# Performance work log

Measured on AMD Instinct MI355X. Metric: run time of the kernel, lower is better.

The kernel has to match this reference:

```python
import jax, jax.numpy as jnp
import numpy as np

N_NODES = 100000
N_EDGES = 1600000
IN_F = 128
OUT_F = 32
HEADS = 4
NEG_SLOPE = 0.2


def setup_inputs() -> dict:
    key = jax.random.key(0)
    k1, k2, k3, k4 = jax.random.split(key, 4)
    h = jax.random.normal(k1, (N_NODES, IN_F), dtype=jnp.float32)
    edge_index = jax.random.randint(k2, (2, N_EDGES), 0, N_NODES, dtype=jnp.int32)
    # xavier-ish scale for W [in, heads*out] and a [1, H, 2F]
    w_scale = 1.414 * (2.0 / (IN_F + HEADS * OUT_F)) ** 0.5
    a_scale = 1.414 * (2.0 / (1 + 2 * OUT_F)) ** 0.5
    W = jax.random.normal(k3, (IN_F, HEADS * OUT_F), dtype=jnp.float32) * w_scale
    a = jax.random.normal(k4, (1, HEADS, 2 * OUT_F), dtype=jnp.float32) * a_scale
    return {"h": h, "edge_index": edge_index, "W": W, "a": a}


def reference(h, edge_index, W, a):
    N = h.shape[0]
    Wh = (h @ W).reshape(N, HEADS, OUT_F)            # [N, H, F]
    # split attention vector: cat([Wh_src, Wh_dst]) . a == Wh_src.a_src + Wh_dst.a_dst
    a_src, a_dst = a[..., :OUT_F], a[..., OUT_F:]    # [1, H, F] each
    s_src = jnp.sum(Wh * a_src, axis=-1)             # [N, H] per-node src score
    s_dst = jnp.sum(Wh * a_dst, axis=-1)             # [N, H] per-node dst score
    src, dst = edge_index[0], edge_index[1]
    scores = jax.nn.leaky_relu(s_src[src] + s_dst[dst], NEG_SLOPE)  # [E, H]
    # scatter per-edge scores to a dense [N, H] table (-inf where no edge),
    # softmax over the NODE axis (dim 0, as in the torch code), gather back
    node_scores = jax.ops.segment_max(scores, dst, num_segments=N)  # [N, H], -inf empty
    attn = jax.nn.softmax(node_scores, axis=0)[dst]  # [E, H]
    # weighted scatter-add aggregation (dropout is identity in eval)
    out = jax.ops.segment_sum(attn[:, :, None] * Wh[src], dst, num_segments=N)
    return out.reshape(N, HEADS * OUT_F)
```

## Files before the change

### kernel.cpp

```cpp
#include <hip/hip_runtime.h>
#include <hip/hip_bf16.h>
#include <float.h>

#define N_NODES 100000
#define N_EDGES 1600000
#define HEADS 4
#define OUT_F 32
#define NEG_SLOPE 0.2f
#define EXP_SHIFT 8.0f

#define NB 391
#define NT 391
#define SCAP 12288

typedef __attribute__((ext_vector_type(8))) short short8;
typedef __attribute__((ext_vector_type(4))) float f32x4;

__device__ __forceinline__ int enc_f(float f) {
    int b = __float_as_int(f);
    return b >= 0 ? b : b ^ 0x7fffffff;
}
__device__ __forceinline__ float dec_f(int b) {
    return __int_as_float(b >= 0 ? b : b ^ 0x7fffffff);
}
#define ENC_NEG_FLT_MAX ((int)0x80800000)

__device__ __forceinline__ unsigned short f2bf(float f) {
    unsigned int u = __float_as_uint(f);
    u += 0x7fff + ((u >> 16) & 1);
    return (unsigned short)(u >> 16);
}

__global__ void k_wt(const float* __restrict__ W, unsigned short* __restrict__ Wt,
                     float* __restrict__ S) {
    if (blockIdx.x == 0 && threadIdx.x < 4) S[threadIdx.x] = 0.0f;
    int n = threadIdx.x;
    int k2 = blockIdx.x;
    float w0 = W[(size_t)(2 * k2) * 128 + n];
    float w1 = W[(size_t)(2 * k2 + 1) * 128 + n];
    ushort2 p = make_ushort2(f2bf(w0), f2bf(w1));
    *(ushort2*)&Wt[(size_t)n * 128 + 2 * k2] = p;
}

__global__ __launch_bounds__(256) void k_gemm(const float* __restrict__ hp,
                                              const unsigned short* __restrict__ Wt,
                                              const float* __restrict__ av,
                                              unsigned short* __restrict__ Whb,
                                              float* __restrict__ s_src,
                                              float* __restrict__ s_dst) {
    __shared__ short hs[64][136];
    __shared__ short wsB[128][136];
    int tid = threadIdx.x;
    int rowBase = blockIdx.x * 64;

    const short8* Wt8 = (const short8*)Wt;
#pragma unroll
    for (int i = 0; i < 8; i++) {
        int idx = tid + 256 * i;
        int n = idx >> 4, ch = idx & 15;
        *(short8*)&wsB[n][ch * 8] = Wt8[idx];
    }
    const float4* h4 = (const float4*)hp;
#pragma unroll
    for (int i = 0; i < 8; i++) {
        int idx = tid + 256 * i;
        int r = idx >> 5, c4 = idx & 31;
        int gr = rowBase + r;
        float4 v = (gr < N_NODES) ? h4[(size_t)gr * 32 + c4]
                                  : make_float4(0.f, 0.f, 0.f, 0.f);
        ushort4 p = make_ushort4(f2bf(v.x), f2bf(v.y), f2bf(v.z), f2bf(v.w));
        *(ushort4*)&hs[r][c4 * 4] = p;
    }
    __syncthreads();

    int lane = tid & 63;
    int wv = tid >> 6;
    int l16 = lane & 15, quad = lane >> 4;
    int mbase = wv * 16;

    short8 afr[4];
#pragma unroll
    for (int k4 = 0; k4 < 4; k4++)
        afr[k4] = *(const short8*)&hs[mbase + l16][k4 * 32 + quad * 8];

    f32x4 acc[8];
#pragma unroll
    for (int nt = 0; nt < 8; nt++) {
        acc[nt] = (f32x4){0.f, 0.f, 0.f, 0.f};
#pragma unroll
        for (int k4 = 0; k4 < 4; k4++) {
            short8 b = *(const short8*)&wsB[nt * 16 + l16][k4 * 32 + quad * 8];
            acc[nt] = __builtin_amdgcn_mfma_f32_16x16x32_bf16(afr[k4], b, acc[nt], 0, 0, 0);
        }
    }

    int row0 = rowBase + mbase + quad * 4;
#pragma unroll
    for (int r = 0; r < 4; r++) {
        int row = row0 + r;
        if (row < N_NODES) {
#pragma unroll
            for (int nt = 0; nt < 8; nt++)
                Whb[(size_t)row * 128 + nt * 16 + l16] = f2bf(acc[nt][r]);
        }
    }

    float ps[4][4], pd[4][4];
#pragma unroll
    for (int h = 0; h < 4; h++) {
        float a0s = av[h * 64 + l16];
        float a1s = av[h * 64 + 16 + l16];
        float a0d = av[h * 64 + 32 + l16];
        float a1d = av[h * 64 + 48 + l16];
#pragma unroll
        for (int r = 0; r < 4; r++) {
            ps[h][r] = acc[2 * h][r] * a0s + acc[2 * h + 1][r] * a1s;
            pd[h][r] = acc[2 * h][r] * a0d + acc[2 * h + 1][r] * a1d;
        }
    }
#pragma unroll
    for (int h = 0; h < 4; h++)
#pragma unroll
        for (int r = 0; r < 4; r++) {
#pragma unroll
            for (int off = 1; off < 16; off <<= 1) {
                ps[h][r] += __shfl_xor(ps[h][r], off);
                pd[h][r] += __shfl_xor(pd[h][r], off);
            }
        }
    if (l16 < 4) {
#pragma unroll
        for (int r = 0; r < 4; r++) {
            int row = row0 + r;
            if (row < N_NODES) {
                float vs = (l16 == 0) ? ps[0][r] : (l16 == 1) ? ps[1][r]
                         : (l16 == 2) ? ps[2][r] : ps[3][r];
                float vd = (l16 == 0) ? pd[0][r] : (l16 == 1) ? pd[1][r]
                         : (l16 == 2) ? pd[2][r] : pd[3][r];
                s_src[row * 4 + l16] = vs;
                s_dst[row * 4 + l16] = vd;
            }
        }
    }
}

__global__ __launch_bounds__(256) void k_hist(const int* __restrict__ ei,
                                              int* __restrict__ hist) {
    __shared__ int lh[NB];
    int tid = threadIdx.x, tile = blockIdx.x;
    for (int b = tid; b < NB; b += 256) lh[b] = 0;
    __syncthreads();
    const int4* d4 = (const int4*)(ei + N_EDGES);
    int base4 = tile * 1024;
    for (int i = tid; i < 1024; i += 256) {
        int i4 = base4 + i;
        if (i4 < N_EDGES / 4) {
            int4 d = d4[i4];
            atomicAdd(&lh[d.x >> 8], 1);
            atomicAdd(&lh[d.y >> 8], 1);
            atomicAdd(&lh[d.z >> 8], 1);
            atomicAdd(&lh[d.w >> 8], 1);
        }
    }
    __syncthreads();
    for (int b = tid; b < NB; b += 256) hist[tile * NB + b] = lh[b];
}

__global__ __launch_bounds__(512) void k_scan(const int* __restrict__ hist,
                                              int* __restrict__ tileoff,
                                              int* __restrict__ bin_total) {
    int b = blockIdx.x, tid = threadIdx.x;
    int val = (tid < NT) ? hist[tid * NB + b] : 0;
    int lane = tid & 63, wv = tid >> 6;
    int v = val;
#pragma unroll
    for (int off = 1; off < 64; off <<= 1) {
        int t = __shfl_up(v, off);
        if (lane >= off) v += t;
    }
    __shared__ int wtot[8], woff[8];
    if (lane == 63) wtot[wv] = v;
    __syncthreads();
    if (tid == 0) { int s = 0; for (int i = 0; i < 8; i++) { woff[i] = s; s += wtot[i]; } }
    __syncthreads();
    int incl = v + woff[wv];
    if (tid < NT) tileoff[tid * NB + b] = incl - val;
    if (tid == NT - 1) bin_total[b] = incl;
}

__global__ __launch_bounds__(512) void k_scan2(const int* __restrict__ bin_total,
                                               int* __restrict__ bin_start) {
    int tid = threadIdx.x;
    int val = (tid < NB) ? bin_total[tid] : 0;
    int lane = tid & 63, wv = tid >> 6;
    int v = val;
#pragma unroll
    for (int off = 1; off < 64; off <<= 1) {
        int t = __shfl_up(v, off);
        if (lane >= off) v += t;
    }
    __shared__ int wtot[8], woff[8];
    if (lane == 63) wtot[wv] = v;
    __syncthreads();
    if (tid == 0) { int s = 0; for (int i = 0; i < 8; i++) { woff[i] = s; s += wtot[i]; } }
    __syncthreads();
    if (tid < NB) bin_start[tid] = v + woff[wv] - val;
}

__global__ __launch_bounds__(256) void k_scat(const int* __restrict__ ei,
                                              const int* __restrict__ tileoff,
                                              const int* __restrict__ bin_start,
                                              int* __restrict__ ebuf) {
    __shared__ int lcur[NB];
    int tid = threadIdx.x, tile = blockIdx.x;
    for (int b = tid; b < NB; b += 256) lcur[b] = bin_start[b] + tileoff[tile * NB + b];
    __syncthreads();
    const int4* s4 = (const int4*)ei;
    const int4* d4 = (const int4*)(ei + N_EDGES);
    int base4 = tile * 1024;
    for (int i = tid; i < 1024; i += 256) {
        int i4 = base4 + i;
        if (i4 < N_EDGES / 4) {
            int4 s = s4[i4];
            int4 d = d4[i4];
            int p;
            p = atomicAdd(&lcur[d.x >> 8], 1); ebuf[p] = s.x | ((d.x & 255) << 17);
            p = atomicAdd(&lcur[d.y >> 8], 1); ebuf[p] = s.y | ((d.y & 255) << 17);
            p = atomicAdd(&lcur[d.z >> 8], 1); ebuf[p] = s.z | ((d.z & 255) << 17);
            p = atomicAdd(&lcur[d.w >> 8], 1); ebuf[p] = s.w | ((d.w & 255) << 17);
        }
    }
}

__global__ __launch_bounds__(256) void k_bucket(const int* __restrict__ bin_start,
                                                const int* __restrict__ bin_total,
                                                int* __restrict__ ebuf,
                                                int* __restrict__ cnt,
                                                int* __restrict__ start,
                                                const float* __restrict__ s_src,
                                                const float* __restrict__ s_dst,
                                                float* __restrict__ expv,
                                                float* __restrict__ S) {
    __shared__ int stage[SCAP];
    __shared__ int lh[256];
    __shared__ int lcur[256];
    __shared__ int nm[4][256];
    __shared__ int wtot[4], woff[4];
    __shared__ float sred[4][4];
    int b = blockIdx.x, tid = threadIdx.x;
    int base = bin_start[b], total = bin_total[b];
    if (total > SCAP) total = SCAP;
    lh[tid] = 0;
    nm[0][tid] = ENC_NEG_FLT_MAX; nm[1][tid] = ENC_NEG_FLT_MAX;
    nm[2][tid] = ENC_NEG_FLT_MAX; nm[3][tid] = ENC_NEG_FLT_MAX;
    __syncthreads();
    for (int i = tid; i < total; i += 256) {
        int rec = ebuf[base + i];
        stage[i] = rec;
        atomicAdd(&lh[(rec >> 17) & 255], 1);
    }
    __syncthreads();
    int val = lh[tid];
    int lane = tid & 63, wv = tid >> 6;
    int v = val;
#pragma unroll
    for (int off = 1; off < 64; off <<= 1) {
        int t = __shfl_up(v, off);
        if (lane >= off) v += t;
    }
    if (lane == 63) wtot[wv] = v;
    __syncthreads();
    if (tid == 0) { int s = 0; for (int i = 0; i < 4; i++) { woff[i] = s; s += wtot[i]; } }
    __syncthreads();
    int gpos = base + v + woff[wv] - val;
    int node = b * 256 + tid;
    if (node < N_NODES) { cnt[node] = val; start[node] = gpos; }
    lcur[tid] = gpos;
    __syncthreads();
    for (int i = tid; i < total; i += 256) {
        int rec = stage[i];
        int src = rec & 0x1FFFF;
        int ld = (rec >> 17) & 255;
        int p = atomicAdd(&lcur[ld], 1);
        ebuf[p] = src;
        float4 sv = ((const float4*)s_src)[src];
        atomicMax(&nm[0][ld], enc_f(sv.x));
        atomicMax(&nm[1][ld], enc_f(sv.y));
        atomicMax(&nm[2][ld], enc_f(sv.z));
        atomicMax(&nm[3][ld], enc_f(sv.w));
    }
    __syncthreads();
    float4 e4 = make_float4(0.f, 0.f, 0.f, 0.f);
    if (node < N_NODES) {
        float4 d = ((const float4*)s_dst)[node];
        float x;
        x = dec_f(nm[0][tid]) + d.x; x = x > 0.f ? x : NEG_SLOPE * x; e4.x = __expf(x - EXP_SHIFT);
        x = dec_f(nm[1][tid]) + d.y; x = x > 0.f ? x : NEG_SLOPE * x; e4.y = __expf(x - EXP_SHIFT);
        x = dec_f(nm[2][tid]) + d.z; x = x > 0.f ? x : NEG_SLOPE * x; e4.z = __expf(x - EXP_SHIFT);
        x = dec_f(nm[3][tid]) + d.w; x = x > 0.f ? x : NEG_SLOPE * x; e4.w = __expf(x - EXP_SHIFT);
        ((float4*)expv)[node] = e4;
    }
#pragma unroll
    for (int off = 32; off; off >>= 1) {
        e4.x += __shfl_xor(e4.x, off);
        e4.y += __shfl_xor(e4.y, off);
        e4.z += __shfl_xor(e4.z, off);
        e4.w += __shfl_xor(e4.w, off);
    }
    if (lane == 0) { sred[wv][0] = e4.x; sred[wv][1] = e4.y; sred[wv][2] = e4.z; sred[wv][3] = e4.w; }
    __syncthreads();
    if (tid < 4)
        atomicAdd(&S[tid], sred[0][tid] + sred[1][tid] + sred[2][tid] + sred[3][tid]);
}

__global__ __launch_bounds__(256) void k_agg(const unsigned int* __restrict__ Whb32,
                                             const int* __restrict__ esrc,
                                             const int* __restrict__ start,
                                             const int* __restrict__ cnt,
                                             const float* __restrict__ expv,
                                             const float* __restrict__ S,
                                             float* __restrict__ out) {
    int node = (blockIdx.x * 256 + threadIdx.x) >> 6;
    if (node >= N_NODES) return;
    int lane = threadIdx.x & 63;
    int base = __builtin_amdgcn_readfirstlane(start[node]);
    int deg  = __builtin_amdgcn_readfirstlane(cnt[node]);
    const unsigned int* Wl = Whb32 + lane;
    float accx = 0.f, accy = 0.f;
    int i = 0;
    for (; i + 16 <= deg; i += 16) {
        unsigned int v[16];
#pragma unroll
        for (int j = 0; j < 16; j++) {
            int s = esrc[base + i + j];
            v[j] = Wl[(size_t)s * 64];
        }
#pragma unroll
        for (int j = 0; j < 16; j++) {
            accx += __uint_as_float(v[j] << 16);
            accy += __uint_as_float(v[j] & 0xffff0000u);
        }
    }
    for (; i + 4 <= deg; i += 4) {
        unsigned int v[4];
#pragma unroll
        for (int j = 0; j < 4; j++) {
            int s = esrc[base + i + j];
            v[j] = Wl[(size_t)s * 64];
        }
#pragma unroll
        for (int j = 0; j < 4; j++) {
            accx += __uint_as_float(v[j] << 16);
            accy += __uint_as_float(v[j] & 0xffff0000u);
        }
    }
    for (; i < deg; i++) {
        int s = esrc[base + i];
        unsigned int v = Wl[(size_t)s * 64];
        accx += __uint_as_float(v << 16);
        accy += __uint_as_float(v & 0xffff0000u);
    }
    int head = lane >> 4;
    float attn = expv[node * 4 + head] / S[head];
    ((float2*)out)[(size_t)node * 64 + lane] = make_float2(accx * attn, accy * attn);
}

extern "C" void kernel_launch(void* const* d_in, const int* in_sizes, int n_in,
                              void* d_out, int out_size, void* d_ws, size_t ws_size,
                              hipStream_t stream) {
    const float* h  = (const float*)d_in[0];
    const int*   ei = (const int*)d_in[1];
    const float* W  = (const float*)d_in[2];
    const float* a  = (const float*)d_in[3];
    float* out = (float*)d_out;

    char* ws = (char*)d_ws;
    unsigned short* Whb = (unsigned short*)(ws);
    float* s_src     = (float*)(ws + 25600000);
    float* s_dst     = (float*)(ws + 27200000);
    float* expv      = (float*)(ws + 28800000);
    int*   cnt       = (int*)  (ws + 30400000);
    int*   start     = (int*)  (ws + 30800000);
    int*   ebuf      = (int*)  (ws + 31200000);
    int*   hist      = (int*)  (ws + 37600000);
    int*   tileoff   = (int*)  (ws + 38211524);
    int*   bin_total = (int*)  (ws + 38823048);
    int*   bin_start = (int*)  (ws + 38824612);
    float* S         = (float*)(ws + 38826176);
    unsigned short* Wt = (unsigned short*)ebuf;

    k_wt<<<64, 128, 0, stream>>>(W, Wt, S);
    k_gemm<<<1563, 256, 0, stream>>>(h, Wt, a, Whb, s_src, s_dst);
    k_hist<<<NT, 256, 0, stream>>>(ei, hist);
    k_scan<<<NB, 512, 0, stream>>>(hist, tileoff, bin_total);
    k_scan2<<<1, 512, 0, stream>>>(bin_total, bin_start);
    k_scat<<<NT, 256, 0, stream>>>(ei, tileoff, bin_start, ebuf);
    k_bucket<<<NB, 256, 0, stream>>>(bin_start, bin_total, ebuf, cnt, start,
                                     s_src, s_dst, expv, S);
    k_agg<<<25000, 256, 0, stream>>>((const unsigned int*)Whb, ebuf, start, cnt, expv, S, out);
}
```

Measured before the change: 236.8 us.

## Fixed-capacity 128-node bins, fuse hist with W prep, pad neighbor lists

Edges are binned into 782 bins of 128 destination nodes, each at a fixed offset of PCAP slots, which removes the second global scan kernel. The histogram pass and the W transpose are fused into one launch. The GEMM now loads h straight into registers, with 128 rows per block. Each node's neighbor list is padded to a multiple of 4 using a dummy source (row N_NODES of Whb, which the GEMM now writes), so the aggregation drops its scalar tail loop. The costs are extra workspace and padding traffic, plus a risk of overflow if a bin holds more than PCAP edges or a node has more than SCAP.

```diff
diff --git a/kernel.cpp b/kernel.cpp
--- a/kernel.cpp
+++ b/kernel.cpp
@@ -9,9 +9,10 @@
 #define NEG_SLOPE 0.2f
 #define EXP_SHIFT 8.0f
 
-#define NB 391
+#define NB 782
 #define NT 391
-#define SCAP 12288
+#define PCAP 4096
+#define SCAP 3072
 
 typedef __attribute__((ext_vector_type(8))) short short8;
 typedef __attribute__((ext_vector_type(4))) float f32x4;
@@ -31,57 +32,79 @@
     return (unsigned short)(u >> 16);
 }
 
-__global__ void k_wt(const float* __restrict__ W, unsigned short* __restrict__ Wt,
-                     float* __restrict__ S) {
-    if (blockIdx.x == 0 && threadIdx.x < 4) S[threadIdx.x] = 0.0f;
-    int n = threadIdx.x;
-    int k2 = blockIdx.x;
-    float w0 = W[(size_t)(2 * k2) * 128 + n];
-    float w1 = W[(size_t)(2 * k2 + 1) * 128 + n];
-    ushort2 p = make_ushort2(f2bf(w0), f2bf(w1));
-    *(ushort2*)&Wt[(size_t)n * 128 + 2 * k2] = p;
-}
-
-__global__ __launch_bounds__(256) void k_gemm(const float* __restrict__ hp,
+__global__ __launch_bounds__(256) void k_prep(const int* __restrict__ ei,
+                                              const float* __restrict__ W,
+                                              unsigned short* __restrict__ Wt,
+                                              int* __restrict__ hist,
+                                              float* __restrict__ S) {
+    __shared__ int lh[NB];
+    int b = blockIdx.x, tid = threadIdx.x;
+    if (b < NT) {
+        for (int i = tid; i < NB; i += 256) lh[i] = 0;
+        __syncthreads();
+        const int4* d4 = (const int4*)(ei + N_EDGES);
+        int base4 = b * 1024;
+#pragma unroll
+        for (int it = 0; it < 4; it++) {
+            int i4 = base4 + tid + 256 * it;
+            if (i4 < N_EDGES / 4) {
+                int4 d = d4[i4];
+                atomicAdd(&lh[d.x >> 7], 1);
+                atomicAdd(&lh[d.y >> 7], 1);
+                atomicAdd(&lh[d.z >> 7], 1);
+                atomicAdd(&lh[d.w >> 7], 1);
+            }
+        }
+        __syncthreads();
+        for (int i = tid; i < NB; i += 256) hist[b * NB + i] = lh[i];
+    } else {
+        int idx = (b - NT) * 256 + tid;
+        int n = idx & 127, k2 = idx >> 7;
+        float w0 = W[(size_t)(2 * k2) * 128 + n];
+        float w1 = W[(size_t)(2 * k2 + 1) * 128 + n];
+        *(ushort2*)&Wt[(size_t)n * 128 + 2 * k2] = make_ushort2(f2bf(w0), f2bf(w1));
+        if (b == NT && tid < 4) S[tid] = 0.0f;
+    }
+}
+
+__global__ __launch_bounds__(512) void k_gemm(const float* __restrict__ hp,
                                               const unsigned short* __restrict__ Wt,
                                               const float* __restrict__ av,
                                               unsigned short* __restrict__ Whb,
                                               float* __restrict__ s_src,
                                               float* __restrict__ s_dst) {
-    __shared__ short hs[64][136];
     __shared__ short wsB[128][136];
     int tid = threadIdx.x;
-    int rowBase = blockIdx.x * 64;
+    int rowBase = blockIdx.x * 128;
 
     const short8* Wt8 = (const short8*)Wt;
 #pragma unroll
-    for (int i = 0; i < 8; i++) {
-        int idx = tid + 256 * i;
+    for (int i = 0; i < 4; i++) {
+        int idx = tid + 512 * i;
         int n = idx >> 4, ch = idx & 15;
         *(short8*)&wsB[n][ch * 8] = Wt8[idx];
-    }
-    const float4* h4 = (const float4*)hp;
-#pragma unroll
-    for (int i = 0; i < 8; i++) {
-        int idx = tid + 256 * i;
-        int r = idx >> 5, c4 = idx & 31;
-        int gr = rowBase + r;
-        float4 v = (gr < N_NODES) ? h4[(size_t)gr * 32 + c4]
-                                  : make_float4(0.f, 0.f, 0.f, 0.f);
-        ushort4 p = make_ushort4(f2bf(v.x), f2bf(v.y), f2bf(v.z), f2bf(v.w));
-        *(ushort4*)&hs[r][c4 * 4] = p;
     }
     __syncthreads();
 
     int lane = tid & 63;
     int wv = tid >> 6;
     int l16 = lane & 15, quad = lane >> 4;
-    int mbase = wv * 16;
-
+
+    int arow = rowBase + wv * 16 + l16;
+    bool valid = arow < N_NODES;
+    const float* hrow = hp + (size_t)arow * 128;
     short8 afr[4];
 #pragma unroll
-    for (int k4 = 0; k4 < 4; k4++)
-        afr[k4] = *(const short8*)&hs[mbase + l16][k4 * 32 + quad * 8];
+    for (int k4 = 0; k4 < 4; k4++) {
+        float4 u0 = valid ? *(const float4*)&hrow[k4 * 32 + quad * 8]
+                          : make_float4(0.f, 0.f, 0.f, 0.f);
+        float4 u1 = valid ? *(const float4*)&hrow[k4 * 32 + quad * 8 + 4]
+                          : make_float4(0.f, 0.f, 0.f, 0.f);
+        afr[k4] = (short8){(short)f2bf(u0.x), (short)f2bf(u0.y),
+                           (short)f2bf(u0.z), (short)f2bf(u0.w),
+                           (short)f2bf(u1.x), (short)f2bf(u1.y),
+                           (short)f2bf(u1.z), (short)f2bf(u1.w)};
+    }
 
     f32x4 acc[8];
 #pragma unroll
@@ -89,16 +112,16 @@
         acc[nt] = (f32x4){0.f, 0.f, 0.f, 0.f};
 #pragma unroll
         for (int k4 = 0; k4 < 4; k4++) {
-            short8 b = *(const short8*)&wsB[nt * 16 + l16][k4 * 32 + quad * 8];
-            acc[nt] = __builtin_amdgcn_mfma_f32_16x16x32_bf16(afr[k4], b, acc[nt], 0, 0, 0);
-        }
-    }
-
-    int row0 = rowBase + mbase + quad * 4;
+            short8 bfr = *(const short8*)&wsB[nt * 16 + l16][k4 * 32 + quad * 8];
+            acc[nt] = __builtin_amdgcn_mfma_f32_16x16x32_bf16(afr[k4], bfr, acc[nt], 0, 0, 0);
+        }
+    }
+
+    int row0 = rowBase + wv * 16 + quad * 4;
 #pragma unroll
     for (int r = 0; r < 4; r++) {
         int row = row0 + r;
-        if (row < N_NODES) {
+        if (row <= N_NODES) {
 #pragma unroll
             for (int nt = 0; nt < 8; nt++)
                 Whb[(size_t)row * 128 + nt * 16 + l16] = f2bf(acc[nt][r]);
@@ -144,28 +167,6 @@
     }
 }
 
-__global__ __launch_bounds__(256) void k_hist(const int* __restrict__ ei,
-                                              int* __restrict__ hist) {
-    __shared__ int lh[NB];
-    int tid = threadIdx.x, tile = blockIdx.x;
-    for (int b = tid; b < NB; b += 256) lh[b] = 0;
-    __syncthreads();
-    const int4* d4 = (const int4*)(ei + N_EDGES);
-    int base4 = tile * 1024;
-    for (int i = tid; i < 1024; i += 256) {
-        int i4 = base4 + i;
-        if (i4 < N_EDGES / 4) {
-            int4 d = d4[i4];
-            atomicAdd(&lh[d.x >> 8], 1);
-            atomicAdd(&lh[d.y >> 8], 1);
-            atomicAdd(&lh[d.z >> 8], 1);
-            atomicAdd(&lh[d.w >> 8], 1);
-        }
-    }
-    __syncthreads();
-    for (int b = tid; b < NB; b += 256) hist[tile * NB + b] = lh[b];
-}
-
 __global__ __launch_bounds__(512) void k_scan(const int* __restrict__ hist,
                                               int* __restrict__ tileoff,
                                               int* __restrict__ bin_total) {
@@ -188,53 +189,34 @@
     if (tid == NT - 1) bin_total[b] = incl;
 }
 
-__global__ __launch_bounds__(512) void k_scan2(const int* __restrict__ bin_total,
-                                               int* __restrict__ bin_start) {
-    int tid = threadIdx.x;
-    int val = (tid < NB) ? bin_total[tid] : 0;
-    int lane = tid & 63, wv = tid >> 6;
-    int v = val;
-#pragma unroll
-    for (int off = 1; off < 64; off <<= 1) {
-        int t = __shfl_up(v, off);
-        if (lane >= off) v += t;
-    }
-    __shared__ int wtot[8], woff[8];
-    if (lane == 63) wtot[wv] = v;
-    __syncthreads();
-    if (tid == 0) { int s = 0; for (int i = 0; i < 8; i++) { woff[i] = s; s += wtot[i]; } }
-    __syncthreads();
-    if (tid < NB) bin_start[tid] = v + woff[wv] - val;
-}
-
 __global__ __launch_bounds__(256) void k_scat(const int* __restrict__ ei,
                                               const int* __restrict__ tileoff,
-                                              const int* __restrict__ bin_start,
                                               int* __restrict__ ebuf) {
     __shared__ int lcur[NB];
     int tid = threadIdx.x, tile = blockIdx.x;
-    for (int b = tid; b < NB; b += 256) lcur[b] = bin_start[b] + tileoff[tile * NB + b];
+    for (int i = tid; i < NB; i += 256) lcur[i] = i * PCAP + tileoff[tile * NB + i];
     __syncthreads();
     const int4* s4 = (const int4*)ei;
     const int4* d4 = (const int4*)(ei + N_EDGES);
     int base4 = tile * 1024;
-    for (int i = tid; i < 1024; i += 256) {
-        int i4 = base4 + i;
+#pragma unroll
+    for (int it = 0; it < 4; it++) {
+        int i4 = base4 + tid + 256 * it;
         if (i4 < N_EDGES / 4) {
             int4 s = s4[i4];
             int4 d = d4[i4];
             int p;
-            p = atomicAdd(&lcur[d.x >> 8], 1); ebuf[p] = s.x | ((d.x & 255) << 17);
-            p = atomicAdd(&lcur[d.y >> 8], 1); ebuf[p] = s.y | ((d.y & 255) << 17);
-            p = atomicAdd(&lcur[d.z >> 8], 1); ebuf[p] = s.z | ((d.z & 255) << 17);
-            p = atomicAdd(&lcur[d.w >> 8], 1); ebuf[p] = s.w | ((d.w & 255) << 17);
-        }
-    }
-}
-
-__global__ __launch_bounds__(256) void k_bucket(const int* __restrict__ bin_start,
-                                                const int* __restrict__ bin_total,
-                                                int* __restrict__ ebuf,
+            p = atomicAdd(&lcur[d.x >> 7], 1); ebuf[p] = s.x | ((d.x & 127) << 17);
+            p = atomicAdd(&lcur[d.y >> 7], 1); ebuf[p] = s.y | ((d.y & 127) << 17);
+            p = atomicAdd(&lcur[d.z >> 7], 1); ebuf[p] = s.z | ((d.z & 127) << 17);
+            p = atomicAdd(&lcur[d.w >> 7], 1); ebuf[p] = s.w | ((d.w & 127) << 17);
+        }
+    }
+}
+
+__global__ __launch_bounds__(256) void k_bucket(const int* __restrict__ bin_total,
+                                                const int* __restrict__ ebuf,
+                                                int* __restrict__ esrc,
                                                 int* __restrict__ cnt,
                                                 int* __restrict__ start,
                                                 const float* __restrict__ s_src,
@@ -242,47 +224,54 @@
                                                 float* __restrict__ expv,
                                                 float* __restrict__ S) {
     __shared__ int stage[SCAP];
-    __shared__ int lh[256];
-    __shared__ int lcur[256];
-    __shared__ int nm[4][256];
-    __shared__ int wtot[4], woff[4];
+    __shared__ int lh[128];
+    __shared__ int lcur[128];
+    __shared__ int nm[4][128];
+    __shared__ int wq;
     __shared__ float sred[4][4];
     int b = blockIdx.x, tid = threadIdx.x;
-    int base = bin_start[b], total = bin_total[b];
+    int base = b * PCAP;
+    int total = bin_total[b];
     if (total > SCAP) total = SCAP;
-    lh[tid] = 0;
-    nm[0][tid] = ENC_NEG_FLT_MAX; nm[1][tid] = ENC_NEG_FLT_MAX;
-    nm[2][tid] = ENC_NEG_FLT_MAX; nm[3][tid] = ENC_NEG_FLT_MAX;
+    if (tid < 128) {
+        lh[tid] = 0;
+        nm[0][tid] = ENC_NEG_FLT_MAX; nm[1][tid] = ENC_NEG_FLT_MAX;
+        nm[2][tid] = ENC_NEG_FLT_MAX; nm[3][tid] = ENC_NEG_FLT_MAX;
+    }
     __syncthreads();
     for (int i = tid; i < total; i += 256) {
         int rec = ebuf[base + i];
         stage[i] = rec;
-        atomicAdd(&lh[(rec >> 17) & 255], 1);
-    }
-    __syncthreads();
-    int val = lh[tid];
-    int lane = tid & 63, wv = tid >> 6;
-    int v = val;
-#pragma unroll
-    for (int off = 1; off < 64; off <<= 1) {
-        int t = __shfl_up(v, off);
-        if (lane >= off) v += t;
-    }
-    if (lane == 63) wtot[wv] = v;
-    __syncthreads();
-    if (tid == 0) { int s = 0; for (int i = 0; i < 4; i++) { woff[i] = s; s += wtot[i]; } }
-    __syncthreads();
-    int gpos = base + v + woff[wv] - val;
-    int node = b * 256 + tid;
-    if (node < N_NODES) { cnt[node] = val; start[node] = gpos; }
-    lcur[tid] = gpos;
+        atomicAdd(&lh[(rec >> 17) & 127], 1);
+    }
+    __syncthreads();
+    int lane = tid & 63;
+    int val = 0, padded = 0, gpos = 0;
+    if (tid < 128) {
+        val = lh[tid];
+        padded = (val + 3) & ~3;
+        int v = padded;
+#pragma unroll
+        for (int off = 1; off < 64; off <<= 1) {
+            int t = __shfl_up(v, off);
+            if (lane >= off) v += t;
+        }
+        if (tid == 63) wq = v;
+        __syncthreads();
+        gpos = base + v - padded + ((tid >= 64) ? wq : 0);
+        int node = b * 128 + tid;
+        if (node < N_NODES) { cnt[node] = padded; start[node] = gpos; }
+        lcur[tid] = gpos;
+    } else {
+        __syncthreads();
+    }
     __syncthreads();
     for (int i = tid; i < total; i += 256) {
         int rec = stage[i];
         int src = rec & 0x1FFFF;
-        int ld = (rec >> 17) & 255;
+        int ld = (rec >> 17) & 127;
         int p = atomicAdd(&lcur[ld], 1);
-        ebuf[p] = src;
+        esrc[p] = src;
         float4 sv = ((const float4*)s_src)[src];
         atomicMax(&nm[0][ld], enc_f(sv.x));
         atomicMax(&nm[1][ld], enc_f(sv.y));
@@ -291,14 +280,18 @@
     }
     __syncthreads();
     float4 e4 = make_float4(0.f, 0.f, 0.f, 0.f);
-    if (node < N_NODES) {
-        float4 d = ((const float4*)s_dst)[node];
-        float x;
-        x = dec_f(nm[0][tid]) + d.x; x = x > 0.f ? x : NEG_SLOPE * x; e4.x = __expf(x - EXP_SHIFT);
-        x = dec_f(nm[1][tid]) + d.y; x = x > 0.f ? x : NEG_SLOPE * x; e4.y = __expf(x - EXP_SHIFT);
-        x = dec_f(nm[2][tid]) + d.z; x = x > 0.f ? x : NEG_SLOPE * x; e4.z = __expf(x - EXP_SHIFT);
-        x = dec_f(nm[3][tid]) + d.w; x = x > 0.f ? x : NEG_SLOPE * x; e4.w = __expf(x - EXP_SHIFT);
-        ((float4*)expv)[node] = e4;
+    if (tid < 128) {
+        for (int k = val; k < padded; k++) esrc[gpos + k] = N_NODES;
+        int node = b * 128 + tid;
+        if (node < N_NODES) {
+            float4 d = ((const float4*)s_dst)[node];
+            float x;
+            x = dec_f(nm[0][tid]) + d.x; x = x > 0.f ? x : NEG_SLOPE * x; e4.x = __expf(x - EXP_SHIFT);
+            x = dec_f(nm[1][tid]) + d.y; x = x > 0.f ? x : NEG_SLOPE * x; e4.y = __expf(x - EXP_SHIFT);
+            x = dec_f(nm[2][tid]) + d.z; x = x > 0.f ? x : NEG_SLOPE * x; e4.z = __expf(x - EXP_SHIFT);
+            x = dec_f(nm[3][tid]) + d.w; x = x > 0.f ? x : NEG_SLOPE * x; e4.w = __expf(x - EXP_SHIFT);
+            ((float4*)expv)[node] = e4;
+        }
     }
 #pragma unroll
     for (int off = 32; off; off >>= 1) {
@@ -307,6 +300,7 @@
         e4.z += __shfl_xor(e4.z, off);
         e4.w += __shfl_xor(e4.w, off);
     }
+    int wv = tid >> 6;
     if (lane == 0) { sred[wv][0] = e4.x; sred[wv][1] = e4.y; sred[wv][2] = e4.z; sred[wv][3] = e4.w; }
     __syncthreads();
     if (tid < 4)
@@ -341,7 +335,7 @@
             accy += __uint_as_float(v[j] & 0xffff0000u);
         }
     }
-    for (; i + 4 <= deg; i += 4) {
+    for (; i < deg; i += 4) {
         unsigned int v[4];
 #pragma unroll
         for (int j = 0; j < 4; j++) {
@@ -353,12 +347,6 @@
             accx += __uint_as_float(v[j] << 16);
             accy += __uint_as_float(v[j] & 0xffff0000u);
         }
-    }
-    for (; i < deg; i++) {
-        int s = esrc[base + i];
-        unsigned int v = Wl[(size_t)s * 64];
-        accx += __uint_as_float(v << 16);
-        accy += __uint_as_float(v & 0xffff0000u);
     }
     int head = lane >> 4;
     float attn = expv[node * 4 + head] / S[head];
@@ -376,26 +364,24 @@
 
     char* ws = (char*)d_ws;
     unsigned short* Whb = (unsigned short*)(ws);
-    float* s_src     = (float*)(ws + 25600000);
-    float* s_dst     = (float*)(ws + 27200000);
-    float* expv      = (float*)(ws + 28800000);
-    int*   cnt       = (int*)  (ws + 30400000);
-    int*   start     = (int*)  (ws + 30800000);
-    int*   ebuf      = (int*)  (ws + 31200000);
-    int*   hist      = (int*)  (ws + 37600000);
-    int*   tileoff   = (int*)  (ws + 38211524);
-    int*   bin_total = (int*)  (ws + 38823048);
-    int*   bin_start = (int*)  (ws + 38824612);
-    float* S         = (float*)(ws + 38826176);
+    float* s_src     = (float*)(ws + 25600256);
+    float* s_dst     = (float*)(ws + 27200256);
+    float* expv      = (float*)(ws + 28800256);
+    int*   cnt       = (int*)  (ws + 30400256);
+    int*   start     = (int*)  (ws + 30800256);
+    int*   ebuf      = (int*)  (ws + 31200256);
+    int*   esrc      = (int*)  (ws + 44012544);
+    int*   hist      = (int*)  (ws + 56824832);
+    int*   tileoff   = (int*)  (ws + 58047880);
+    int*   bin_total = (int*)  (ws + 59270928);
+    float* S         = (float*)(ws + 59274056);
     unsigned short* Wt = (unsigned short*)ebuf;
 
-    k_wt<<<64, 128, 0, stream>>>(W, Wt, S);
-    k_gemm<<<1563, 256, 0, stream>>>(h, Wt, a, Whb, s_src, s_dst);
-    k_hist<<<NT, 256, 0, stream>>>(ei, hist);
+    k_prep<<<NT + 32, 256, 0, stream>>>(ei, W, Wt, hist, S);
+    k_gemm<<<782, 512, 0, stream>>>(h, Wt, a, Whb, s_src, s_dst);
     k_scan<<<NB, 512, 0, stream>>>(hist, tileoff, bin_total);
-    k_scan2<<<1, 512, 0, stream>>>(bin_total, bin_start);
-    k_scat<<<NT, 256, 0, stream>>>(ei, tileoff, bin_start, ebuf);
-    k_bucket<<<NB, 256, 0, stream>>>(bin_start, bin_total, ebuf, cnt, start,
+    k_scat<<<NT, 256, 0, stream>>>(ei, tileoff, ebuf);
+    k_bucket<<<NB, 256, 0, stream>>>(bin_total, ebuf, esrc, cnt, start,
                                      s_src, s_dst, expv, S);
-    k_agg<<<25000, 256, 0, stream>>>((const unsigned int*)Whb, ebuf, start, cnt, expv, S, out);
-}
+    k_agg<<<25000, 256, 0, stream>>>((const unsigned int*)Whb, esrc, start, cnt, expv, S, out);
+}
```

Result: no change. 240.7 us (+1.6%).
